# Performance work log

Measured on AMD Instinct MI355X. Metric: run time of the kernel, lower is better.

## Reference

```python
import jax, jax.numpy as jnp
import numpy as np

B, S, C = 64, 512, 1000

def setup_inputs() -> dict:
    key = jax.random.key(0)
    k1, k2 = jax.random.split(key)
    # probabilities in (0,1); add small eps to keep log finite
    output = jax.random.uniform(k1, (B, S, C), dtype=jnp.float32, minval=1e-6, maxval=1.0)
    target = jax.random.randint(k2, (B, S), 0, C, dtype=jnp.int64)
    return {"output": output, "target": target}

def reference(output, target):
    # loss = sum_{i,j} -log(output[i, j, target[i, j]])  (scalar)
    picked = jnp.take_along_axis(output, target[..., None].astype(jnp.int32), axis=-1)[..., 0]  # [B,S]
    return -jnp.sum(jnp.log(picked))
```

## Files before the change

kernel.cpp:

```cpp
#include <hip/hip_runtime.h>

#define B_DIM 64
#define S_DIM 512
#define C_DIM 1000
#define N_TOTAL (B_DIM * S_DIM)
#define NBLOCKS 128
#define NTHREADS 256

__global__ __launch_bounds__(NTHREADS) void loss_partial_kernel(
    const float* __restrict__ out,
    const int*   __restrict__ tgt,
    float*       __restrict__ partials)
{
    int idx = blockIdx.x * NTHREADS + threadIdx.x;
    float acc = 0.0f;
    if (idx < N_TOTAL) {
        int t = tgt[idx];
        float v = out[(long long)idx * C_DIM + t];
        acc = -logf(v);
    }

    #pragma unroll
    for (int off = 32; off > 0; off >>= 1)
        acc += __shfl_down(acc, off, 64);

    __shared__ float smem[NTHREADS / 64];
    int wave = threadIdx.x >> 6;
    if ((threadIdx.x & 63) == 0) smem[wave] = acc;
    __syncthreads();

    if (threadIdx.x == 0) {
        float s = 0.0f;
        #pragma unroll
        for (int w = 0; w < NTHREADS / 64; ++w) s += smem[w];
        partials[blockIdx.x] = s;
    }
}

__global__ __launch_bounds__(128) void loss_final_kernel(
    const float* __restrict__ partials,
    float*       __restrict__ out)
{
    float acc = (threadIdx.x < NBLOCKS) ? partials[threadIdx.x] : 0.0f;

    #pragma unroll
    for (int off = 32; off > 0; off >>= 1)
        acc += __shfl_down(acc, off, 64);

    __shared__ float smem[2];
    int wave = threadIdx.x >> 6;
    if ((threadIdx.x & 63) == 0) smem[wave] = acc;
    __syncthreads();

    if (threadIdx.x == 0) {
        out[0] = smem[0] + smem[1];
    }
}

extern "C" void kernel_launch(void* const* d_in, const int* in_sizes, int n_in,
                              void* d_out, int out_size, void* d_ws, size_t ws_size,
                              hipStream_t stream) {
    const float* out_probs = (const float*)d_in[0];
    const int*   target    = (const int*)d_in[1];
    float* loss = (float*)d_out;
    float* partials = (float*)d_ws;

    loss_partial_kernel<<<NBLOCKS, NTHREADS, 0, stream>>>(out_probs, target, partials);
    loss_final_kernel<<<1, 128, 0, stream>>>(partials, loss);
}
```

Before: 10.89 us.

## Fuse partial and final reduction into one cooperative kernel with grid sync

Replaces the two-kernel reduction with a single cooperative launch that computes per-block partials, does a grid-wide sync, then has block 0 finish the sum. The grid becomes 256 blocks of 128 threads, and logf is swapped for the fast __logf intrinsic. The aim is to drop the second kernel launch and its inter-kernel gap. In exchange it pays for a cooperative launch and a grid barrier, which can cost as much as a launch on AMD.

```diff
diff --git a/kernel.cpp b/kernel.cpp
--- a/kernel.cpp
+++ b/kernel.cpp
@@ -1,70 +1,68 @@
 #include <hip/hip_runtime.h>
+#include <hip/hip_cooperative_groups.h>
 
-#define B_DIM 64
-#define S_DIM 512
+namespace cg = cooperative_groups;
+
 #define C_DIM 1000
-#define N_TOTAL (B_DIM * S_DIM)
-#define NBLOCKS 128
-#define NTHREADS 256
+#define N_TOTAL 32768
+#define NB 256
+#define NT 128
 
-__global__ __launch_bounds__(NTHREADS) void loss_partial_kernel(
-    const float* __restrict__ out,
+__global__ __launch_bounds__(NT) void fused_loss_kernel(
+    const float* __restrict__ probs,
     const int*   __restrict__ tgt,
-    float*       __restrict__ partials)
-{
-    int idx = blockIdx.x * NTHREADS + threadIdx.x;
-    float acc = 0.0f;
-    if (idx < N_TOTAL) {
-        int t = tgt[idx];
-        float v = out[(long long)idx * C_DIM + t];
-        acc = -logf(v);
-    }
+    float*       __restrict__ loss,
+    float*       __restrict__ partials
+){
+    const int tid = threadIdx.x;
+    const int idx = blockIdx.x * NT + tid;
+
+    int   t = tgt[idx];
+    float v = probs[(long long)idx * C_DIM + t];
+    float acc = -__logf(v);
 
     #pragma unroll
     for (int off = 32; off > 0; off >>= 1)
         acc += __shfl_down(acc, off, 64);
 
-    __shared__ float smem[NTHREADS / 64];
-    int wave = threadIdx.x >> 6;
-    if ((threadIdx.x & 63) == 0) smem[wave] = acc;
+    __shared__ float smem[NT / 64];
+    if ((tid & 63) == 0) smem[tid >> 6] = acc;
     __syncthreads();
-
-    if (threadIdx.x == 0) {
+    if (tid == 0) {
         float s = 0.0f;
         #pragma unroll
-        for (int w = 0; w < NTHREADS / 64; ++w) s += smem[w];
+        for (int w = 0; w < NT / 64; ++w) s += smem[w];
         partials[blockIdx.x] = s;
     }
-}
 
-__global__ __launch_bounds__(128) void loss_final_kernel(
-    const float* __restrict__ partials,
-    float*       __restrict__ out)
-{
-    float acc = (threadIdx.x < NBLOCKS) ? partials[threadIdx.x] : 0.0f;
+    cg::this_grid().sync();
 
-    #pragma unroll
-    for (int off = 32; off > 0; off >>= 1)
-        acc += __shfl_down(acc, off, 64);
-
-    __shared__ float smem[2];
-    int wave = threadIdx.x >> 6;
-    if ((threadIdx.x & 63) == 0) smem[wave] = acc;
-    __syncthreads();
-
-    if (threadIdx.x == 0) {
-        out[0] = smem[0] + smem[1];
+    if (blockIdx.x == 0) {
+        float a = partials[tid] + partials[tid + NT];
+        #pragma unroll
+        for (int off = 32; off > 0; off >>= 1)
+            a += __shfl_down(a, off, 64);
+        __shared__ float smem2[NT / 64];
+        if ((tid & 63) == 0) smem2[tid >> 6] = a;
+        __syncthreads();
+        if (tid == 0) {
+            float s = 0.0f;
+            #pragma unroll
+            for (int w = 0; w < NT / 64; ++w) s += smem2[w];
+            loss[0] = s;
+        }
     }
 }
 
 extern "C" void kernel_launch(void* const* d_in, const int* in_sizes, int n_in,
                               void* d_out, int out_size, void* d_ws, size_t ws_size,
                               hipStream_t stream) {
-    const float* out_probs = (const float*)d_in[0];
-    const int*   target    = (const int*)d_in[1];
-    float* loss = (float*)d_out;
+    const float* probs = (const float*)d_in[0];
+    const int*   tgt   = (const int*)d_in[1];
+    float* loss     = (float*)d_out;
     float* partials = (float*)d_ws;
 
-    loss_partial_kernel<<<NBLOCKS, NTHREADS, 0, stream>>>(out_probs, target, partials);
-    loss_final_kernel<<<1, 128, 0, stream>>>(partials, loss);
+    void* args[] = { (void*)&probs, (void*)&tgt, (void*)&loss, (void*)&partials };
+    hipLaunchCooperativeKernel((const void*)fused_loss_kernel,
+                               dim3(NB), dim3(NT), args, 0, stream);
 }
```

Result: slower. 38.55 us (+253.9%).
